# Kernel optimization log

Hardware: AMD Instinct MI355X
Metric: run time of the kernel (lower is better)

## Reference

```python
import jax, jax.numpy as jnp
import numpy as np

N, E, F_IN, DIM, HEADS = 16384, 262144, 128, 64, 4
HID = DIM * HEADS  # 256
NEG = 0.2


def _lin(k, fan_in, fan_out):
    kw, kb = jax.random.split(k)
    s = 1.0 / np.sqrt(fan_in)
    return (jax.random.uniform(kw, (fan_in, fan_out), jnp.float32, -s, s),
            jax.random.uniform(kb, (fan_out,), jnp.float32, -s, s))


def setup_inputs() -> dict:
    key = jax.random.key(0)
    ks = jax.random.split(key, 20)
    x = jax.random.normal(ks[0], (N, F_IN), jnp.float32)
    edge_index = jax.random.randint(ks[1], (2, E), 0, N, jnp.int32)
    Win, b_in = _lin(ks[2], F_IN, DIM)
    Wskip, bskip = _lin(ks[3], DIM, HID)
    # conv1: in=DIM, out per head=DIM, heads=HEADS, concat -> HID
    Wl1, _ = _lin(ks[4], DIM, HID)
    Wr1, _ = _lin(ks[5], DIM, HID)
    att1 = jax.random.normal(ks[6], (HEADS, DIM), jnp.float32) * 0.1
    b1 = jnp.zeros((HID,), jnp.float32)
    # conv2: in=HID, out=HID, heads=1, concat=False
    Wl2, _ = _lin(ks[7], HID, HID)
    Wr2, _ = _lin(ks[8], HID, HID)
    att2 = jax.random.normal(ks[9], (1, HID), jnp.float32) * 0.1
    b2 = jnp.zeros((HID,), jnp.float32)
    # conv3: in=HID, out=HID, heads=1, concat=False
    Wl3, _ = _lin(ks[10], HID, HID)
    Wr3, _ = _lin(ks[11], HID, HID)
    att3 = jax.random.normal(ks[12], (1, HID), jnp.float32) * 0.1
    b3 = jnp.zeros((HID,), jnp.float32)
    Wm1, bm1 = _lin(ks[13], HID, DIM)
    Wm2, bm2 = _lin(ks[14], DIM, DIM)
    Wm3, bm3 = _lin(ks[15], DIM, 1)
    return dict(x=x, edge_index=edge_index, Win=Win, b_in=b_in,
                Wskip=Wskip, bskip=bskip,
                Wl1=Wl1, Wr1=Wr1, att1=att1, b1=b1,
                Wl2=Wl2, Wr2=Wr2, att2=att2, b2=b2,
                Wl3=Wl3, Wr3=Wr3, att3=att3, b3=b3,
                Wm1=Wm1, bm1=bm1, Wm2=Wm2, bm2=bm2, Wm3=Wm3, bm3=bm3)


def gatv2(x, src, dst, Wl, Wr, att, b, concat):
    # PyG GATv2Conv: x_l = lin_l(x)[src], x_r = lin_r(x)[dst]
    n = x.shape[0]
    H, D = att.shape
    xl = (x @ Wl).reshape(n, H, D)
    xr = (x @ Wr).reshape(n, H, D)
    e = jax.nn.leaky_relu(xl[src] + xr[dst], NEG)          # [E, H, D]
    logits = jnp.einsum('ehd,hd->eh', e, att)              # [E, H]
    m = jax.ops.segment_max(logits, dst, num_segments=n)   # per-dst softmax
    alpha = jnp.exp(logits - m[dst])
    denom = jax.ops.segment_sum(alpha, dst, num_segments=n)
    alpha = alpha / denom[dst]
    out = jax.ops.segment_sum(alpha[:, :, None] * xl[src], dst, num_segments=n)
    out = out.reshape(n, H * D) if concat else out.mean(axis=1)
    return out + b


def reference(x, edge_index, Win, b_in, Wskip, bskip,
              Wl1, Wr1, att1, b1, Wl2, Wr2, att2, b2,
              Wl3, Wr3, att3, b3, Wm1, bm1, Wm2, bm2, Wm3, bm3):
    n = x.shape[0]
    # add self loops (GATv2Conv default add_self_loops=True)
    loop = jnp.arange(n, dtype=edge_index.dtype)
    src = jnp.concatenate([edge_index[0], loop])
    dst = jnp.concatenate([edge_index[1], loop])

    h = jax.nn.relu(x @ Win + b_in)                         # [N, DIM]
    out1 = jax.nn.relu(gatv2(h, src, dst, Wl1, Wr1, att1, b1, True))
    out1 = out1 + (h @ Wskip + bskip)                       # [N, HID]
    out2 = jax.nn.relu(gatv2(out1, src, dst, Wl2, Wr2, att2, b2, False))
    out2 = out2 + out1
    out3 = jax.nn.relu(gatv2(out2, src, dst, Wl3, Wr3, att3, b3, False))
    out3 = out3 + out2
    out = jax.nn.relu(out3 @ Wm1 + bm1)
    out = jax.nn.relu(out @ Wm2 + bm2)
    out = out @ Wm3 + bm3                                   # [N, 1]
    return out.reshape(-1)
```

## Files before the change

### kernel.cpp

```cpp
#include <hip/hip_runtime.h>
#include <cstdint>
#include <cstddef>

#define N_NODES 16384
#define E_EDGES 262144
#define FIN     128
#define DIM     64
#define HID     256
#define NEG     0.2f

typedef _Float16 h8 __attribute__((ext_vector_type(8)));
typedef _Float16 h4 __attribute__((ext_vector_type(4)));
typedef _Float16 h2 __attribute__((ext_vector_type(2)));
typedef float    f32x4 __attribute__((ext_vector_type(4)));
typedef float    f32x2 __attribute__((ext_vector_type(2)));

__global__ __launch_bounds__(256) void hist_kernel(const int* __restrict__ dst,
                                                   int* __restrict__ cnt) {
    int i = blockIdx.x * 256 + threadIdx.x;
    if (i < E_EDGES) atomicAdd(&cnt[dst[i]], 1);
}

__global__ __launch_bounds__(256) void csr_scan_kernel(const int* __restrict__ cnt,
                                                       int* __restrict__ offs,
                                                       int* __restrict__ cursor) {
    __shared__ int wsum[4];
    int tid = threadIdx.x, lane = tid & 63, w = tid >> 6;
    int base = tid * 64;
    const int4* c4 = (const int4*)(cnt + base);
    int4 v[16];
    int s = 0;
#pragma unroll
    for (int i = 0; i < 16; ++i) {
        v[i] = c4[i];
        s += v[i].x + v[i].y + v[i].z + v[i].w;
    }
    int scan = s;
#pragma unroll
    for (int off = 1; off < 64; off <<= 1) {
        int t = __shfl_up(scan, off);
        if (lane >= off) scan += t;
    }
    if (lane == 63) wsum[w] = scan;
    __syncthreads();
    int wbase = 0;
#pragma unroll
    for (int i = 0; i < 4; ++i) if (i < w) wbase += wsum[i];
    int run = wbase + (scan - s);
#pragma unroll
    for (int i = 0; i < 16; ++i) {
        int4 o;
        o.x = run;
        o.y = o.x + v[i].x;
        o.z = o.y + v[i].y;
        o.w = o.z + v[i].z;
        *(int4*)(offs + base + 4 * i) = o;
        *(int4*)(cursor + base + 4 * i) = o;
        run = o.w + v[i].w;
    }
    if (tid == 255) offs[N_NODES] = run;
}

__global__ __launch_bounds__(256) void scatter_kernel(const int* __restrict__ src,
                                                      const int* __restrict__ dst,
                                                      int* __restrict__ cursor,
                                                      int* __restrict__ esrc) {
    int i = blockIdx.x * 256 + threadIdx.x;
    if (i < E_EDGES) {
        int p = atomicAdd(&cursor[dst[i]], 1);
        esrc[p] = src[i];
    }
}

struct PackJob { const float* W; _Float16* dst; int Ksrc, Nsrc, NT, colOff; };
struct PackJobs { PackJob j[10]; };

__global__ __launch_bounds__(256) void pack_all_kernel(PackJobs jobs, int* __restrict__ cnt) {
    int i = blockIdx.x * 256 + threadIdx.x;
    if (blockIdx.y == 10) {
        if (i < N_NODES) cnt[i] = 0;
        return;
    }
    PackJob jb = jobs.j[blockIdx.y];
    if (i < jb.Ksrc * jb.Nsrc) {
        int k = i / jb.Nsrc, n = i % jb.Nsrc;
        jb.dst[((size_t)(k >> 3) * jb.NT + jb.colOff + n) * 8 + (k & 7)] = (_Float16)jb.W[i];
    }
}

template<int K, bool RELU, bool O16, bool IN32>
__global__ __launch_bounds__(64) void mfma_n64_kernel(const void* __restrict__ Av,
                                                      const _Float16* __restrict__ Wp,
                                                      const float* __restrict__ bias,
                                                      void* __restrict__ outv) {
    int lane = threadIdx.x;
    int rowBase = blockIdx.x * 64;
    int l15 = lane & 15, l4 = lane >> 4;

    f32x4 acc[4][4] = {};
#pragma unroll
    for (int ks = 0; ks < K / 32; ++ks) {
        h8 af[4], bf[4];
#pragma unroll
        for (int mi = 0; mi < 4; ++mi) {
            if constexpr (IN32) {
                const float* ap = (const float*)Av + (size_t)(rowBase + mi * 16 + l15) * K + ks * 32 + l4 * 8;
                float4 a0 = *(const float4*)ap;
                float4 a1 = *(const float4*)(ap + 4);
                h8 v;
                v[0] = (_Float16)a0.x; v[1] = (_Float16)a0.y;
                v[2] = (_Float16)a0.z; v[3] = (_Float16)a0.w;
                v[4] = (_Float16)a1.x; v[5] = (_Float16)a1.y;
                v[6] = (_Float16)a1.z; v[7] = (_Float16)a1.w;
                af[mi] = v;
            } else {
                af[mi] = *(const h8*)((const _Float16*)Av + (size_t)(rowBase + mi * 16 + l15) * K + ks * 32 + l4 * 8);
            }
        }
#pragma unroll
        for (int ni = 0; ni < 4; ++ni)
            bf[ni] = *(const h8*)(Wp + ((size_t)(ks * 4 + l4) * 64 + ni * 16 + l15) * 8);
#pragma unroll
        for (int mi = 0; mi < 4; ++mi)
#pragma unroll
            for (int ni = 0; ni < 4; ++ni)
                acc[mi][ni] = __builtin_amdgcn_mfma_f32_16x16x32_f16(af[mi], bf[ni], acc[mi][ni], 0, 0, 0);
    }
#pragma unroll
    for (int mi = 0; mi < 4; ++mi)
#pragma unroll
        for (int ni = 0; ni < 4; ++ni) {
            int c = ni * 16 + l15;
            float bv = bias[c];
#pragma unroll
            for (int q = 0; q < 4; ++q) {
                int r = rowBase + mi * 16 + l4 * 4 + q;
                float v = acc[mi][ni][q] + bv;
                if (RELU) v = fmaxf(v, 0.f);
                if constexpr (O16) ((_Float16*)outv)[(size_t)r * 64 + c] = (_Float16)v;
                else               ((float*)outv)[(size_t)r * 64 + c] = v;
            }
        }
}

template<int K>
__global__ __launch_bounds__(256) void mfma_gemm_kernel(const _Float16* __restrict__ A,
                                                        const _Float16* __restrict__ Wp,
                                                        int NT,
                                                        _Float16* __restrict__ o16a,
                                                        _Float16* __restrict__ o16b,
                                                        float* __restrict__ o32,
                                                        const float* __restrict__ bias) {
    int tid = threadIdx.x;
    int lane = tid & 63, wid = tid >> 6;
    int wm = wid >> 1, wn = wid & 1;
    int rowBase = blockIdx.x * 128 + wm * 64;
    int colBase = blockIdx.y * 128 + wn * 64;
    int l15 = lane & 15, l4 = lane >> 4;

    f32x4 acc[4][4] = {};
#pragma unroll
    for (int ks = 0; ks < K / 32; ++ks) {
        h8 af[4], bf[4];
#pragma unroll
        for (int mi = 0; mi < 4; ++mi)
            af[mi] = *(const h8*)(A + (size_t)(rowBase + mi * 16 + l15) * K + ks * 32 + l4 * 8);
#pragma unroll
        for (int ni = 0; ni < 4; ++ni)
            bf[ni] = *(const h8*)(Wp + ((size_t)(ks * 4 + l4) * NT + colBase + ni * 16 + l15) * 8);
#pragma unroll
        for (int mi = 0; mi < 4; ++mi)
#pragma unroll
            for (int ni = 0; ni < 4; ++ni)
                acc[mi][ni] = __builtin_amdgcn_mfma_f32_16x16x32_f16(af[mi], bf[ni], acc[mi][ni], 0, 0, 0);
    }

    int seg = colBase >> 8;
    int cbase = colBase & 255;
    if (o32 != nullptr && seg == 2) {
#pragma unroll
        for (int mi = 0; mi < 4; ++mi)
#pragma unroll
            for (int ni = 0; ni < 4; ++ni) {
                int c = cbase + ni * 16 + l15;
                float bv = bias[c];
#pragma unroll
                for (int q = 0; q < 4; ++q) {
                    int r = rowBase + mi * 16 + l4 * 4 + q;
                    o32[(size_t)r * 256 + c] = acc[mi][ni][q] + bv;
                }
            }
    } else {
        _Float16* o = (seg == 0) ? o16a : o16b;
#pragma unroll
        for (int mi = 0; mi < 4; ++mi)
#pragma unroll
            for (int ni = 0; ni < 4; ++ni) {
                int c = cbase + ni * 16 + l15;
#pragma unroll
                for (int q = 0; q < 4; ++q) {
                    int r = rowBase + mi * 16 + l4 * 4 + q;
                    o[(size_t)r * 256 + c] = (_Float16)acc[mi][ni][q];
                }
            }
    }
}

template<int H, int OMODE>
__global__ __launch_bounds__(256) void gat_agg_kernel(const _Float16* __restrict__ xl,
                                                      const _Float16* __restrict__ xr,
                                                      const float* __restrict__ att,
                                                      const float* __restrict__ bias,
                                                      const float* __restrict__ resid,
                                                      const int* __restrict__ offs,
                                                      const int* __restrict__ esrc,
                                                      float* __restrict__ out,
                                                      _Float16* __restrict__ out16) {
    int tid = threadIdx.x;
    int wid = tid >> 6;
    int lane = tid & 63;
    int node = blockIdx.x * 4 + wid;
    int g  = lane >> 4;
    int li = lane & 15;

    h2 xrv[8];
    {
        const h8* xp = (const h8*)(xr + ((size_t)node << 8) + (li << 4));
        h8 a0 = xp[0], a1 = xp[1];
#pragma unroll
        for (int i = 0; i < 4; ++i) { xrv[i][0] = a0[2 * i]; xrv[i][1] = a0[2 * i + 1]; }
#pragma unroll
        for (int i = 0; i < 4; ++i) { xrv[4 + i][0] = a1[2 * i]; xrv[4 + i][1] = a1[2 * i + 1]; }
    }
    h2 attv[8];
    {
        const float4* ap = (const float4*)(att + (li << 4));
#pragma unroll
        for (int i = 0; i < 4; ++i) {
            float4 a = ap[i];
            attv[2 * i][0] = (_Float16)a.x; attv[2 * i][1] = (_Float16)a.y;
            attv[2 * i + 1][0] = (_Float16)a.z; attv[2 * i + 1][1] = (_Float16)a.w;
        }
    }
    const h2 negc = { (_Float16)NEG, (_Float16)NEG };

    int dbase = (li << 4) + (g << 2);
    float4 bv = *(const float4*)(bias + dbase);
    float4 rv = *(const float4*)(resid + ((size_t)node << 8) + dbase);

    float m = -1e30f, s = 0.f;
    f32x2 acc2[8];
#pragma unroll
    for (int i = 0; i < 8; ++i) acc2[i] = (f32x2){0.f, 0.f};

    int e0 = offs[node];
    int total = offs[node + 1] - e0 + 1;

    auto gather = [&](int srcn, h2* hv) {
        const h8* xp = (const h8*)(xl + ((size_t)srcn << 8) + (li << 4));
        h8 a0 = xp[0], a1 = xp[1];
#pragma unroll
        for (int i = 0; i < 4; ++i) { hv[i][0] = a0[2 * i]; hv[i][1] = a0[2 * i + 1]; }
#pragma unroll
        for (int i = 0; i < 4; ++i) { hv[4 + i][0] = a1[2 * i]; hv[4 + i][1] = a1[2 * i + 1]; }
    };
    auto logit = [&](const h2* hv) -> float {
        float part = 0.f;
#pragma unroll
        for (int i = 0; i < 8; ++i) {
            h2 sum = hv[i] + xrv[i];
            h2 lr = __builtin_elementwise_max(sum, sum * negc);
            part = __builtin_amdgcn_fdot2(lr, attv[i], part, false);
        }
        part += __shfl_xor(part, 1);
        part += __shfl_xor(part, 2);
        if constexpr (H == 1) {
            part += __shfl_xor(part, 4);
            part += __shfl_xor(part, 8);
        }
        return part;
    };

    int vi = g;
    for (; vi + 4 < total; vi += 8) {
        int sA = (vi == 0) ? node : esrc[e0 + vi - 1];
        int sB = esrc[e0 + vi + 3];
        h2 hA[8], hB[8];
        gather(sA, hA);
        gather(sB, hB);
        float lpA = logit(hA);
        float lpB = logit(hB);
        float mn = fmaxf(m, fmaxf(lpA, lpB));
        float c  = __expf(m - mn);
        float pA = __expf(lpA - mn);
        float pB = __expf(lpB - mn);
        s = s * c + pA + pB;
#pragma unroll
        for (int i = 0; i < 8; ++i) {
            f32x2 t = acc2[i] * c;
            t[0] = fmaf(pA, (float)hA[i][0], t[0]);
            t[1] = fmaf(pA, (float)hA[i][1], t[1]);
            t[0] = fmaf(pB, (float)hB[i][0], t[0]);
            t[1] = fmaf(pB, (float)hB[i][1], t[1]);
            acc2[i] = t;
        }
        m = mn;
    }
    for (; vi < total; vi += 4) {
        int srcn = (vi == 0) ? node : esrc[e0 + vi - 1];
        h2 hA[8];
        gather(srcn, hA);
        float lp = logit(hA);
        float mn = fmaxf(m, lp);
        float c = __expf(m - mn);
        float p = __expf(lp - mn);
        s = s * c + p;
#pragma unroll
        for (int i = 0; i < 8; ++i) {
            f32x2 t = acc2[i] * c;
            t[0] = fmaf(p, (float)hA[i][0], t[0]);
            t[1] = fmaf(p, (float)hA[i][1], t[1]);
            acc2[i] = t;
        }
        m = mn;
    }

#pragma unroll
    for (int mask = 16; mask <= 32; mask <<= 1) {
        float m2 = __shfl_xor(m, mask);
        float s2 = __shfl_xor(s, mask);
        float M = fmaxf(m, m2);
        float c1 = __expf(m - M);
        float c2 = __expf(m2 - M);
        s = s * c1 + s2 * c2;
#pragma unroll
        for (int i = 0; i < 8; ++i) {
            float ax = __shfl_xor(acc2[i][0], mask);
            float ay = __shfl_xor(acc2[i][1], mask);
            acc2[i][0] = acc2[i][0] * c1 + ax * c2;
            acc2[i][1] = acc2[i][1] * c1 + ay * c2;
        }
        m = M;
    }

    float inv = 1.f / s;
    float a0, a1v, a2, a3;
    if (g == 0)      { a0 = acc2[0][0]; a1v = acc2[0][1]; a2 = acc2[1][0]; a3 = acc2[1][1]; }
    else if (g == 1) { a0 = acc2[2][0]; a1v = acc2[2][1]; a2 = acc2[3][0]; a3 = acc2[3][1]; }
    else if (g == 2) { a0 = acc2[4][0]; a1v = acc2[4][1]; a2 = acc2[5][0]; a3 = acc2[5][1]; }
    else             { a0 = acc2[6][0]; a1v = acc2[6][1]; a2 = acc2[7][0]; a3 = acc2[7][1]; }
    float o0 = fmaxf(a0 * inv + bv.x, 0.f) + rv.x;
    float o1 = fmaxf(a1v * inv + bv.y, 0.f) + rv.y;
    float o2 = fmaxf(a2 * inv + bv.z, 0.f) + rv.z;
    float o3 = fmaxf(a3 * inv + bv.w, 0.f) + rv.w;
    if constexpr (OMODE != 2) {
        float4 ov = make_float4(o0, o1, o2, o3);
        *(float4*)(out + ((size_t)node << 8) + dbase) = ov;
    }
    if constexpr (OMODE != 0) {
        h4 hv;
        hv[0] = (_Float16)o0; hv[1] = (_Float16)o1;
        hv[2] = (_Float16)o2; hv[3] = (_Float16)o3;
        *(h4*)(out16 + ((size_t)node << 8) + dbase) = hv;
    }
}

__global__ __launch_bounds__(256) void mlp_head_kernel(const _Float16* __restrict__ A,
                                                       const _Float16* __restrict__ Wm1p,
                                                       const float* __restrict__ bm1,
                                                       const _Float16* __restrict__ Wm2p,
                                                       const float* __restrict__ bm2,
                                                       const float* __restrict__ Wm3,
                                                       const float* __restrict__ bm3,
                                                       float* __restrict__ out) {
    __shared__ _Float16 t1s[4][16][72];
    int tid = threadIdx.x;
    int lane = tid & 63, wid = tid >> 6;
    int rowBase = blockIdx.x * 64 + wid * 16;
    int l15 = lane & 15, l4 = lane >> 4;

    f32x4 acc[4] = {};
#pragma unroll
    for (int ks = 0; ks < 8; ++ks) {
        h8 af = *(const h8*)(A + (size_t)(rowBase + l15) * 256 + ks * 32 + l4 * 8);
        h8 bf[4];
#pragma unroll
        for (int ni = 0; ni < 4; ++ni)
            bf[ni] = *(const h8*)(Wm1p + ((size_t)(ks * 4 + l4) * 64 + ni * 16 + l15) * 8);
#pragma unroll
        for (int ni = 0; ni < 4; ++ni)
            acc[ni] = __builtin_amdgcn_mfma_f32_16x16x32_f16(af, bf[ni], acc[ni], 0, 0, 0);
    }
#pragma unroll
    for (int ni = 0; ni < 4; ++ni) {
        int c = ni * 16 + l15;
        float bv = bm1[c];
#pragma unroll
        for (int q = 0; q < 4; ++q)
            t1s[wid][l4 * 4 + q][c] = (_Float16)fmaxf(acc[ni][q] + bv, 0.f);
    }

    f32x4 acc2[4] = {};
#pragma unroll
    for (int ks = 0; ks < 2; ++ks) {
        h8 af = *(const h8*)&t1s[wid][l15][ks * 32 + l4 * 8];
        h8 bf[4];
#pragma unroll
        for (int ni = 0; ni < 4; ++ni)
            bf[ni] = *(const h8*)(Wm2p + ((size_t)(ks * 4 + l4) * 64 + ni * 16 + l15) * 8);
#pragma unroll
        for (int ni = 0; ni < 4; ++ni)
            acc2[ni] = __builtin_amdgcn_mfma_f32_16x16x32_f16(af, bf[ni], acc2[ni], 0, 0, 0);
    }

    float b3 = bm3[0];
    float b2v[4], w3v[4];
#pragma unroll
    for (int ni = 0; ni < 4; ++ni) {
        b2v[ni] = bm2[ni * 16 + l15];
        w3v[ni] = Wm3[ni * 16 + l15];
    }
#pragma unroll
    for (int q = 0; q < 4; ++q) {
        float part = 0.f;
#pragma unroll
        for (int ni = 0; ni < 4; ++ni)
            part += fmaxf(acc2[ni][q] + b2v[ni], 0.f) * w3v[ni];
        part += __shfl_xor(part, 1);
        part += __shfl_xor(part, 2);
        part += __shfl_xor(part, 4);
        part += __shfl_xor(part, 8);
        if (l15 == 0)
            out[rowBase + l4 * 4 + q] = part + b3;
    }
}

extern "C" void kernel_launch(void* const* d_in, const int* in_sizes, int n_in,
                              void* d_out, int out_size, void* d_ws, size_t ws_size,
                              hipStream_t stream) {
    const float* x     = (const float*)d_in[0];
    const int*   ei    = (const int*)d_in[1];
    const float* Win   = (const float*)d_in[2];
    const float* b_in  = (const float*)d_in[3];
    const float* Wskip = (const float*)d_in[4];
    const float* bskip = (const float*)d_in[5];
    const float* Wl1   = (const float*)d_in[6];
    const float* Wr1   = (const float*)d_in[7];
    const float* att1  = (const float*)d_in[8];
    const float* b1    = (const float*)d_in[9];
    const float* Wl2   = (const float*)d_in[10];
    const float* Wr2   = (const float*)d_in[11];
    const float* att2  = (const float*)d_in[12];
    const float* b2    = (const float*)d_in[13];
    const float* Wl3   = (const float*)d_in[14];
    const float* Wr3   = (const float*)d_in[15];
    const float* att3  = (const float*)d_in[16];
    const float* b3    = (const float*)d_in[17];
    const float* Wm1   = (const float*)d_in[18];
    const float* bm1   = (const float*)d_in[19];
    const float* Wm2   = (const float*)d_in[20];
    const float* bm2   = (const float*)d_in[21];
    const float* Wm3   = (const float*)d_in[22];
    const float* bm3   = (const float*)d_in[23];

    char* p = (char*)d_ws;
    auto alloc = [&](size_t bytes) { char* r = p; p += (bytes + 255) & ~(size_t)255; return r; };
    const size_t NN = N_NODES;
    float*    skip = (float*)alloc(NN * 256 * 4);
    float*    out1 = (float*)alloc(NN * 256 * 4);
    _Float16* o116 = (_Float16*)alloc(NN * 256 * 2);
    _Float16* o216 = (_Float16*)alloc(NN * 256 * 2);
    _Float16* o316 = o116;
    _Float16* h16  = (_Float16*)alloc(NN * 64 * 2);
    _Float16* xl16 = (_Float16*)alloc(NN * 256 * 2);
    _Float16* xr16 = (_Float16*)alloc(NN * 256 * 2);
    _Float16* Wp1  = (_Float16*)alloc((size_t)64 * 768 * 2);
    _Float16* Wp2  = (_Float16*)alloc((size_t)256 * 512 * 2);
    _Float16* Wp3  = (_Float16*)alloc((size_t)256 * 512 * 2);
    _Float16* Winp = (_Float16*)alloc((size_t)128 * 64 * 2);
    _Float16* Wm1p = (_Float16*)alloc((size_t)256 * 64 * 2);
    _Float16* Wm2p = (_Float16*)alloc((size_t)64 * 64 * 2);
    int* cnt    = (int*)alloc(N_NODES * 4);
    int* offs   = (int*)alloc((N_NODES + 1) * 4);
    int* cursor = (int*)alloc(N_NODES * 4);
    int* esrc   = (int*)alloc(E_EDGES * 4);

    const int* src = ei;
    const int* dst = ei + E_EDGES;

    PackJobs jobs = {{
        { Wl1,   Wp1,  64,  256, 768, 0   },
        { Wr1,   Wp1,  64,  256, 768, 256 },
        { Wskip, Wp1,  64,  256, 768, 512 },
        { Wl2,   Wp2,  256, 256, 512, 0   },
        { Wr2,   Wp2,  256, 256, 512, 256 },
        { Wl3,   Wp3,  256, 256, 512, 0   },
        { Wr3,   Wp3,  256, 256, 512, 256 },
        { Win,   Winp, 128, 64,  64,  0   },
        { Wm1,   Wm1p, 256, 64,  64,  0   },
        { Wm2,   Wm2p, 64,  64,  64,  0   },
    }};
    pack_all_kernel<<<dim3(256, 11), 256, 0, stream>>>(jobs, cnt);

    hist_kernel<<<E_EDGES / 256, 256, 0, stream>>>(dst, cnt);
    csr_scan_kernel<<<1, 256, 0, stream>>>(cnt, offs, cursor);
    scatter_kernel<<<E_EDGES / 256, 256, 0, stream>>>(src, dst, cursor, esrc);

    mfma_n64_kernel<128, true, true, true><<<N_NODES / 64, 64, 0, stream>>>(x, Winp, b_in, h16);

    mfma_gemm_kernel<64><<<dim3(128, 6), 256, 0, stream>>>(h16, Wp1, 768, xl16, xr16, skip, bskip);
    gat_agg_kernel<4, 1><<<N_NODES / 4, 256, 0, stream>>>(xl16, xr16, att1, b1, skip, offs, esrc, out1, o116);

    mfma_gemm_kernel<256><<<dim3(128, 4), 256, 0, stream>>>(o116, Wp2, 512, xl16, xr16, nullptr, nullptr);
    gat_agg_kernel<1, 1><<<N_NODES / 4, 256, 0, stream>>>(xl16, xr16, att2, b2, out1, offs, esrc, skip , o216);

    mfma_gemm_kernel<256><<<dim3(128, 4), 256, 0, stream>>>(o216, Wp3, 512, xl16, xr16, nullptr, nullptr);
    gat_agg_kernel<1, 2><<<N_NODES / 4, 256, 0, stream>>>(xl16, xr16, att3, b3, skip , offs, esrc, nullptr, o316);

    mlp_head_kernel<<<N_NODES / 64, 256, 0, stream>>>(o316, Wm1p, bm1, Wm2p, bm2, Wm3, bm3, (float*)d_out);
}
```

Baseline: 199.6 us.

## Prefetch next edge indices, use lazy softmax rescaling, split dot-product chains

The aggregation loop now loads the source indices for the next iteration before gathering the current rows, which hides the dependent index-load latency. The online softmax skips rescaling the accumulators unless the new max exceeds the running max by a threshold (8), saving an exp and 16 multiplies per step. The attention logit dot product is split into two independent accumulation chains to shorten the dependency chain. The lazy rescale lets exp terms grow up to e^8, and the clamped prefetch indices read one harmless extra element near the array end.

Measured after the change: 195.3 us. -2.2%, faster.

```diff
diff --git a/kernel.cpp b/kernel.cpp
--- a/kernel.cpp
+++ b/kernel.cpp
@@ -265,13 +265,17 @@
         for (int i = 0; i < 4; ++i) { hv[4 + i][0] = a1[2 * i]; hv[4 + i][1] = a1[2 * i + 1]; }
     };
     auto logit = [&](const h2* hv) -> float {
-        float part = 0.f;
-#pragma unroll
-        for (int i = 0; i < 8; ++i) {
+        float p0 = 0.f, p1 = 0.f;
+#pragma unroll
+        for (int i = 0; i < 4; ++i) {
             h2 sum = hv[i] + xrv[i];
             h2 lr = __builtin_elementwise_max(sum, sum * negc);
-            part = __builtin_amdgcn_fdot2(lr, attv[i], part, false);
-        }
+            p0 = __builtin_amdgcn_fdot2(lr, attv[i], p0, false);
+            h2 sum2 = hv[4 + i] + xrv[4 + i];
+            h2 lr2 = __builtin_elementwise_max(sum2, sum2 * negc);
+            p1 = __builtin_amdgcn_fdot2(lr2, attv[4 + i], p1, false);
+        }
+        float part = p0 + p1;
         part += __shfl_xor(part, 1);
         part += __shfl_xor(part, 2);
         if constexpr (H == 1) {
@@ -282,47 +286,83 @@
     };
 
     int vi = g;
+    int sA = 0, sB = 0;
+    if (vi + 4 < total) {
+        sA = (vi == 0) ? node : esrc[e0 + vi - 1];
+        sB = esrc[e0 + vi + 3];
+    }
     for (; vi + 4 < total; vi += 8) {
-        int sA = (vi == 0) ? node : esrc[e0 + vi - 1];
-        int sB = esrc[e0 + vi + 3];
+        int nvi = vi + 8;
+        int ia = e0 + nvi - 1; if (ia > E_EDGES - 1) ia = E_EDGES - 1;
+        int ib = e0 + nvi + 3; if (ib > E_EDGES - 1) ib = E_EDGES - 1;
+        int sA2 = esrc[ia];
+        int sB2 = esrc[ib];
+
         h2 hA[8], hB[8];
         gather(sA, hA);
         gather(sB, hB);
         float lpA = logit(hA);
         float lpB = logit(hB);
-        float mn = fmaxf(m, fmaxf(lpA, lpB));
-        float c  = __expf(m - mn);
-        float pA = __expf(lpA - mn);
-        float pB = __expf(lpB - mn);
-        s = s * c + pA + pB;
-#pragma unroll
-        for (int i = 0; i < 8; ++i) {
-            f32x2 t = acc2[i] * c;
-            t[0] = fmaf(pA, (float)hA[i][0], t[0]);
-            t[1] = fmaf(pA, (float)hA[i][1], t[1]);
-            t[0] = fmaf(pB, (float)hB[i][0], t[0]);
-            t[1] = fmaf(pB, (float)hB[i][1], t[1]);
-            acc2[i] = t;
-        }
-        m = mn;
+        float mx = fmaxf(lpA, lpB);
+        if (mx > m + 8.f) {
+            float c  = __expf(m - mx);
+            float pA = __expf(lpA - mx);
+            float pB = __expf(lpB - mx);
+            s = s * c + pA + pB;
+#pragma unroll
+            for (int i = 0; i < 8; ++i) {
+                f32x2 t = acc2[i] * c;
+                t[0] = fmaf(pA, (float)hA[i][0], t[0]);
+                t[1] = fmaf(pA, (float)hA[i][1], t[1]);
+                t[0] = fmaf(pB, (float)hB[i][0], t[0]);
+                t[1] = fmaf(pB, (float)hB[i][1], t[1]);
+                acc2[i] = t;
+            }
+            m = mx;
+        } else {
+            float pA = __expf(lpA - m);
+            float pB = __expf(lpB - m);
+            s += pA + pB;
+#pragma unroll
+            for (int i = 0; i < 8; ++i) {
+                f32x2 t = acc2[i];
+                t[0] = fmaf(pA, (float)hA[i][0], t[0]);
+                t[1] = fmaf(pA, (float)hA[i][1], t[1]);
+                t[0] = fmaf(pB, (float)hB[i][0], t[0]);
+                t[1] = fmaf(pB, (float)hB[i][1], t[1]);
+                acc2[i] = t;
+            }
+        }
+        sA = sA2; sB = sB2;
     }
     for (; vi < total; vi += 4) {
         int srcn = (vi == 0) ? node : esrc[e0 + vi - 1];
         h2 hA[8];
         gather(srcn, hA);
         float lp = logit(hA);
-        float mn = fmaxf(m, lp);
-        float c = __expf(m - mn);
-        float p = __expf(lp - mn);
-        s = s * c + p;
-#pragma unroll
-        for (int i = 0; i < 8; ++i) {
-            f32x2 t = acc2[i] * c;
-            t[0] = fmaf(p, (float)hA[i][0], t[0]);
-            t[1] = fmaf(p, (float)hA[i][1], t[1]);
-            acc2[i] = t;
-        }
-        m = mn;
+        if (lp > m + 8.f) {
+            float c = __expf(m - lp);
+            float p = 1.f;
+            s = s * c + p;
+#pragma unroll
+            for (int i = 0; i < 8; ++i) {
+                f32x2 t = acc2[i] * c;
+                t[0] = fmaf(p, (float)hA[i][0], t[0]);
+                t[1] = fmaf(p, (float)hA[i][1], t[1]);
+                acc2[i] = t;
+            }
+            m = lp;
+        } else {
+            float p = __expf(lp - m);
+            s += p;
+#pragma unroll
+            for (int i = 0; i < 8; ++i) {
+                f32x2 t = acc2[i];
+                t[0] = fmaf(p, (float)hA[i][0], t[0]);
+                t[1] = fmaf(p, (float)hA[i][1], t[1]);
+                acc2[i] = t;
+            }
+        }
     }
 
 #pragma unroll
```
